# Kernel optimization log

Hardware: AMD Instinct MI355X
Metric: run time of the kernel (lower is better)

Reference implementation:

```python
import jax, jax.numpy as jnp
import numpy as np

EPS = 1e-10


def setup_inputs() -> dict:
    key = jax.random.key(0)
    ks = jax.random.split(key, 8)
    N, C, H, W = 32, 512, 14, 14
    D, HID = 2048, 256
    s1 = 1.0 / np.sqrt(C + D)
    s2 = 1.0 / np.sqrt(HID)
    return {
        "local_feature": jax.random.normal(ks[0], (N, C, H, W), jnp.float32),
        "global_feature": jax.random.normal(ks[1], (N, D, 1, 1), jnp.float32),
        "W1": jax.random.normal(ks[2], (C + D, HID), jnp.float32) * s1,
        "b1": jnp.zeros((HID,), jnp.float32),
        "W2": jax.random.normal(ks[3], (HID, HID), jnp.float32) * s2,
        "b2": jnp.zeros((HID,), jnp.float32),
        "W3": jax.random.normal(ks[4], (HID, 1), jnp.float32) * s2,
        "b3": jnp.zeros((1,), jnp.float32),
    }


def reference(local_feature, global_feature, W1, b1, W2, b2, W3, b3):
    # Vectorized form of DMIEstimator.calculate_mi (the per-sample Python loop
    # collapsed into one batched pass with a block-diagonal negative mask).
    N, C, H, W = local_feature.shape
    hw = H * W
    nhw = N * hw
    D = global_feature.shape[1]

    lf = jnp.transpose(local_feature, (0, 2, 3, 1)).reshape(nhw, C)   # [nhw, C]
    gf = global_feature[:, :, 0, 0]                                   # [N, D]

    # combined = cat([global, local], -1); split the first Linear accordingly
    # so the [N*nhw, C+D] concat tensor is never materialized.
    h_loc = lf @ W1[D:]                        # [nhw, HID]
    h_glb = gf @ W1[:D] + b1                   # [N, HID]
    h1 = jax.nn.relu(h_glb[:, None, :] + h_loc[None, :, :])  # [N, nhw, HID]
    h2 = jax.nn.relu(h1 @ W2 + b2)                            # [N, nhw, HID]
    scores = (h2 @ W3)[..., 0] + b3[0]                        # [N, nhw]

    mx = jnp.max(scores, axis=1, keepdims=True)               # [N, 1]
    ex = jnp.exp(scores - mx)

    # negatives for sample i exclude its own hw block [hw*i, hw*(i+1))
    own = (jnp.arange(nhw)[None, :] // hw) == jnp.arange(N)[:, None]  # [N, nhw]
    neg_mean = jnp.where(own, 0.0, ex).sum(axis=1) / (nhw - hw) + EPS  # [N]

    # positive (diagonal) block of scores: scores[i, hw*i : hw*(i+1)]
    pos = scores.reshape(N, N, hw)[jnp.arange(N), jnp.arange(N)]       # [N, hw]

    mi = pos - mx - jnp.log(neg_mean)[:, None]                         # [N, hw]
    return mi.reshape(N, H, W)
```

## Files before the change

### kernel.cpp

```cpp
#include <hip/hip_runtime.h>
#include <math.h>

#define NB   32
#define CC   512
#define DD   2048
#define HWP  196
#define NHW  6272
#define HID  256

typedef _Float16 h8 __attribute__((ext_vector_type(8)));
typedef _Float16 h4 __attribute__((ext_vector_type(4)));
typedef float    f4 __attribute__((ext_vector_type(4)));
union F4H8 { f4 f; h8 h; };

__device__ __forceinline__ int fragIdx(int j, int k) {
    return ((j >> 6) << 14) + (((k >> 5) * 4 + ((j & 63) >> 4)) << 9)
         + (((((k >> 3) & 3) << 4) + (j & 15)) << 3) + (k & 7);
}

__global__ __launch_bounds__(1024) void prep_kernel(const float* __restrict__ lf,
                                                    const float* __restrict__ gf,
                                                    const float* __restrict__ W1,
                                                    const float* __restrict__ b1,
                                                    const float* __restrict__ W2,
                                                    _Float16* __restrict__ g16,
                                                    _Float16* __restrict__ W2F,
                                                    _Float16* __restrict__ W1F,
                                                    _Float16* __restrict__ lf16T) {
    int bid = blockIdx.x, tid = threadIdx.x;
    if (bid < 32) {
        __shared__ float sP[4][HID];
        int i = bid, k = tid & 255, rc = tid >> 8;
        const float* g = gf + (size_t)i * DD;
        int r0 = rc * 512;
        float acc = 0.f;
        #pragma unroll 8
        for (int r = 0; r < 512; r++)
            acc = fmaf(g[r0 + r], W1[(size_t)(r0 + r) * HID + k], acc);
        sP[rc][k] = acc;
        __syncthreads();
        if (tid < HID)
            g16[(size_t)i * HID + tid] =
                (_Float16)(b1[tid] + sP[0][tid] + sP[1][tid] + sP[2][tid] + sP[3][tid]);
    } else if (bid < 56) {
        int tg = (bid - 32) * 1024 + tid;
        if (tg < 8192) {
            int t = tg, F = t >> 6, l = t & 63;
            int k2t = F >> 3, ks = F & 7;
            int kb = ks * 32 + (l >> 4) * 8;
            int n  = k2t * 16 + (l & 15);
            _Float16* o = W2F + (size_t)t * 8;
            #pragma unroll
            for (int j = 0; j < 8; j++) o[j] = (_Float16)W2[(size_t)(kb + j) * HID + n];
        } else {
            int t = tg - 8192, F = t >> 6, l = t & 63;
            int k2t = F >> 4, ks = F & 15;
            int kb = ks * 32 + (l >> 4) * 8;
            int n  = k2t * 16 + (l & 15);
            const float* W1c = W1 + (size_t)DD * HID;
            _Float16* o = W1F + (size_t)t * 8;
            #pragma unroll
            for (int j = 0; j < 8; j++) o[j] = (_Float16)W1c[(size_t)(kb + j) * HID + n];
        }
    } else {
        __shared__ _Float16 sT[64][HWP + 4];
        int b = bid - 56;
        int n = b >> 1, half = b & 1;
        for (int cb = 0; cb < 4; cb++) {
            int c0 = half * 256 + cb * 64;
            for (int task = tid; task < 64 * 49; task += 1024) {
                int c = task / 49, f = task - c * 49;
                f4 v = *(const f4*)&lf[((size_t)n * CC + c0 + c) * HWP + f * 4];
                h4 o = { (_Float16)v.x, (_Float16)v.y, (_Float16)v.z, (_Float16)v.w };
                *(h4*)&sT[c][f * 4] = o;
            }
            __syncthreads();
            for (int task = tid; task < HWP * 8; task += 1024) {
                int p = task >> 3, ch = task & 7;
                h8 o;
                #pragma unroll
                for (int cc = 0; cc < 8; cc++) o[cc] = sT[ch * 8 + cc][p];
                *(h8*)&lf16T[((size_t)(n * HWP + p)) * CC + c0 + ch * 8] = o;
            }
            __syncthreads();
        }
    }
}

__global__ __launch_bounds__(256, 2) void hlocF_kernel(const _Float16* __restrict__ lf16T,
                                                       const _Float16* __restrict__ W1F,
                                                       _Float16* __restrict__ hF) {
    __shared__ _Float16 sLf[32][CC + 16];
    int tid = threadIdx.x;
    int w = tid >> 6, l = tid & 63, quad = l >> 4, ln = l & 15;
    int j0 = blockIdx.x * 32;
    int khalf = blockIdx.y;

    #pragma unroll
    for (int s = 0; s < 8; s++) {
        int y = s * 256 + tid;
        int row = y >> 6, col = (y & 63) * 8;
        h8 v = *(const h8*)&lf16T[(size_t)(j0 + row) * CC + col];
        *(h8*)&sLf[row][col] = v;
    }

    F4H8 Af[32];
    {
        const f4* src = (const f4*)W1F + l;
        #pragma unroll
        for (int mt = 0; mt < 2; mt++)
            #pragma unroll
            for (int ks = 0; ks < 16; ks++)
                Af[mt * 16 + ks].f = src[(size_t)((khalf * 8 + w * 2 + mt) * 16 + ks) * 64];
    }
    __syncthreads();

    f4 acc[4] = {};
    #pragma unroll
    for (int ks = 0; ks < 16; ks++) {
        h8 bF[2];
        #pragma unroll
        for (int nt = 0; nt < 2; nt++)
            bF[nt] = *(const h8*)&sLf[nt * 16 + ln][ks * 32 + quad * 8];
        #pragma unroll
        for (int mt = 0; mt < 2; mt++)
            #pragma unroll
            for (int nt = 0; nt < 2; nt++)
                acc[mt * 2 + nt] = __builtin_amdgcn_mfma_f32_16x16x32_f16(Af[mt * 16 + ks].h, bF[nt], acc[mt * 2 + nt], 0, 0, 0);
    }

    #pragma unroll
    for (int mt = 0; mt < 2; mt++)
        #pragma unroll
        for (int nt = 0; nt < 2; nt++)
            #pragma unroll
            for (int r = 0; r < 4; r++) {
                int j  = j0 + nt * 16 + ln;
                int k2 = khalf * 128 + w * 32 + mt * 16 + quad * 4 + r;
                hF[fragIdx(j, k2)] = (_Float16)acc[mt * 2 + nt][r];
            }
}

__global__ __launch_bounds__(256, 2) void score_kernel(const _Float16* __restrict__ hF,
                                                       const _Float16* __restrict__ g16,
                                                       const _Float16* __restrict__ W2F,
                                                       const float* __restrict__ b2,
                                                       const float* __restrict__ W3,
                                                       const float* __restrict__ b3,
                                                       float* __restrict__ scores) {
    __shared__ _Float16 sA[64 * HID];
    __shared__ float sRed[64][4];
    int tid = threadIdx.x, w = tid >> 6, l = tid & 63, quad = l >> 4, ln = l & 15;
    int bid = blockIdx.x;
    int i = bid & 31, jt = bid >> 5;

    F4H8 Af[32];
    {
        const f4* src = (const f4*)W2F + l;
        #pragma unroll
        for (int mt = 0; mt < 4; mt++)
            #pragma unroll
            for (int ks = 0; ks < 8; ks++)
                Af[mt * 8 + ks].f = src[(size_t)((w * 4 + mt) * 8 + ks) * 64];
    }

    {
        const _Float16* hbase = hF + (size_t)jt * 16384;
        const _Float16* gbase = g16 + (size_t)i * HID;
        h8 z = {};
        #pragma unroll
        for (int s = 0; s < 8; s++) {
            int y = s * 256 + tid;
            h8 hv = *(const h8*)&hbase[y * 8];
            h8 gq = *(const h8*)&gbase[s * 32 + ((tid >> 4) & 3) * 8];
            h8 hz = __builtin_elementwise_max(hv + gq, z);
            *(h8*)&sA[y * 8] = hz;
        }
    }
    __syncthreads();

    f4 acc[16];
    #pragma unroll
    for (int mt = 0; mt < 4; mt++) {
        f4 bv = *(const f4*)&b2[w * 64 + mt * 16 + quad * 4];
        #pragma unroll
        for (int nt = 0; nt < 4; nt++) acc[mt * 4 + nt] = bv;
    }

    #pragma unroll
    for (int ks = 0; ks < 8; ks++) {
        #pragma unroll
        for (int nt = 0; nt < 4; nt++) {
            h8 hz = *(const h8*)&sA[(ks * 4 + nt) * 512 + l * 8];
            #pragma unroll
            for (int mt = 0; mt < 4; mt++)
                acc[mt * 4 + nt] = __builtin_amdgcn_mfma_f32_16x16x32_f16(Af[mt * 8 + ks].h, hz, acc[mt * 4 + nt], 0, 0, 0);
        }
    }

    #pragma unroll
    for (int nt = 0; nt < 4; nt++) {
        float s = 0.f;
        #pragma unroll
        for (int mt = 0; mt < 4; mt++) {
            f4 w3v = *(const f4*)&W3[w * 64 + mt * 16 + quad * 4];
            s += fmaxf(acc[mt * 4 + nt][0], 0.f) * w3v.x
               + fmaxf(acc[mt * 4 + nt][1], 0.f) * w3v.y
               + fmaxf(acc[mt * 4 + nt][2], 0.f) * w3v.z
               + fmaxf(acc[mt * 4 + nt][3], 0.f) * w3v.w;
        }
        s += __shfl_xor(s, 16, 64);
        s += __shfl_xor(s, 32, 64);
        if (quad == 0) sRed[nt * 16 + ln][w] = s;
    }
    __syncthreads();
    if (tid < 64) {
        f4 v = *(const f4*)&sRed[tid][0];
        scores[(size_t)i * NHW + jt * 64 + tid] = v.x + v.y + v.z + v.w + b3[0];
    }
}

__global__ __launch_bounds__(1024) void reduce_kernel(const float* __restrict__ scores,
                                                      float* __restrict__ out) {
    int i = blockIdx.x, tid = threadIdx.x;
    const float* row = scores + (size_t)i * NHW;
    const f4* row4 = (const f4*)row;
    __shared__ float sW[16], sW2[16], sval[2];
    float mx = -1e30f;
    for (int q = tid; q < 1568; q += 1024) {
        f4 v = row4[q];
        mx = fmaxf(mx, fmaxf(fmaxf(v.x, v.y), fmaxf(v.z, v.w)));
    }
    #pragma unroll
    for (int off = 32; off > 0; off >>= 1) mx = fmaxf(mx, __shfl_down(mx, off, 64));
    if ((tid & 63) == 0) sW[tid >> 6] = mx;
    __syncthreads();
    if (tid == 0) {
        float m = sW[0];
        for (int c = 1; c < 16; c++) m = fmaxf(m, sW[c]);
        sval[0] = m;
    }
    __syncthreads();
    mx = sval[0];
    int q0 = i * 49, q1 = q0 + 49;
    float tot = 0.f, ownv = 0.f;
    for (int q = tid; q < 1568; q += 1024) {
        f4 v = row4[q];
        float e = expf(v.x - mx) + expf(v.y - mx) + expf(v.z - mx) + expf(v.w - mx);
        tot += e;
        if (q >= q0 && q < q1) ownv += e;
    }
    #pragma unroll
    for (int off = 32; off > 0; off >>= 1) {
        tot  += __shfl_down(tot, off, 64);
        ownv += __shfl_down(ownv, off, 64);
    }
    if ((tid & 63) == 0) { sW[tid >> 6] = tot; sW2[tid >> 6] = ownv; }
    __syncthreads();
    if (tid == 0) {
        float t = 0.f, o = 0.f;
        for (int c = 0; c < 16; c++) { t += sW[c]; o += sW2[c]; }
        float neg_mean = (t - o) / (float)(NHW - HWP) + 1e-10f;
        sval[1] = mx + logf(neg_mean);
    }
    __syncthreads();
    float sub = sval[1];
    if (tid < HWP) out[(size_t)i * HWP + tid] = row[i * HWP + tid] - sub;
}

extern "C" void kernel_launch(void* const* d_in, const int* in_sizes, int n_in,
                              void* d_out, int out_size, void* d_ws, size_t ws_size,
                              hipStream_t stream) {
    const float* lf = (const float*)d_in[0];
    const float* gf = (const float*)d_in[1];
    const float* W1 = (const float*)d_in[2];
    const float* b1 = (const float*)d_in[3];
    const float* W2 = (const float*)d_in[4];
    const float* b2 = (const float*)d_in[5];
    const float* W3 = (const float*)d_in[6];
    const float* b3 = (const float*)d_in[7];
    float* out = (float*)d_out;

    char* ws = (char*)d_ws;
    _Float16* hF     = (_Float16*)ws;
    _Float16* g16    = (_Float16*)(ws + 3211264);
    _Float16* W2F    = (_Float16*)(ws + 3227648);
    _Float16* W1F    = (_Float16*)(ws + 3358720);
    _Float16* lf16T  = (_Float16*)(ws + 3620864);
    float*    scores = (float*)   (ws + 10043392);

    hipLaunchKernelGGL(prep_kernel, dim3(120), dim3(1024), 0, stream,
                       lf, gf, W1, b1, W2, g16, W2F, W1F, lf16T);
    hipLaunchKernelGGL(hlocF_kernel, dim3(196, 2), dim3(256), 0, stream, lf16T, W1F, hF);
    hipLaunchKernelGGL(score_kernel, dim3(3136), dim3(256), 0, stream,
                       hF, g16, W2F, b2, W3, b3, scores);
    hipLaunchKernelGGL(reduce_kernel, dim3(NB), dim3(1024), 0, stream, scores, out);
}
```

Before: 145.2 us.

## Split prep work into many small blocks and defer global GEMV reduction

The prep kernel goes from 120 blocks of 1024 threads to 864 blocks of 256 threads. The global-feature GEMV is split into 16 K-chunks per sample that write partial sums to a workspace buffer. An extra block column in the hlocF kernel then sums those partials with b1 into g16. The transpose work is also split per 64-channel slice, and score_kernel's launch bounds are raised to ask for 4 blocks per SM. The aim is to spread the serial prep phase across more CUs; the cost is an extra partial-sum buffer and possible register pressure in score_kernel.

```diff
diff --git a/kernel.cpp b/kernel.cpp
--- a/kernel.cpp
+++ b/kernel.cpp
@@ -18,32 +18,25 @@
          + (((((k >> 3) & 3) << 4) + (j & 15)) << 3) + (k & 7);
 }
 
-__global__ __launch_bounds__(1024) void prep_kernel(const float* __restrict__ lf,
-                                                    const float* __restrict__ gf,
-                                                    const float* __restrict__ W1,
-                                                    const float* __restrict__ b1,
-                                                    const float* __restrict__ W2,
-                                                    _Float16* __restrict__ g16,
-                                                    _Float16* __restrict__ W2F,
-                                                    _Float16* __restrict__ W1F,
-                                                    _Float16* __restrict__ lf16T) {
+__global__ __launch_bounds__(256) void prep_kernel(const float* __restrict__ lf,
+                                                   const float* __restrict__ gf,
+                                                   const float* __restrict__ W1,
+                                                   const float* __restrict__ W2,
+                                                   float* __restrict__ hpart,
+                                                   _Float16* __restrict__ W2F,
+                                                   _Float16* __restrict__ W1F,
+                                                   _Float16* __restrict__ lf16T) {
     int bid = blockIdx.x, tid = threadIdx.x;
-    if (bid < 32) {
-        __shared__ float sP[4][HID];
-        int i = bid, k = tid & 255, rc = tid >> 8;
-        const float* g = gf + (size_t)i * DD;
-        int r0 = rc * 512;
+    if (bid < 512) {
+        int i = bid >> 4, ky = bid & 15, k = tid;
+        const float* g = gf + (size_t)i * DD + ky * 128;
+        const float* w = W1 + (size_t)(ky * 128) * HID + k;
         float acc = 0.f;
         #pragma unroll 8
-        for (int r = 0; r < 512; r++)
-            acc = fmaf(g[r0 + r], W1[(size_t)(r0 + r) * HID + k], acc);
-        sP[rc][k] = acc;
-        __syncthreads();
-        if (tid < HID)
-            g16[(size_t)i * HID + tid] =
-                (_Float16)(b1[tid] + sP[0][tid] + sP[1][tid] + sP[2][tid] + sP[3][tid]);
-    } else if (bid < 56) {
-        int tg = (bid - 32) * 1024 + tid;
+        for (int r = 0; r < 128; r++) acc = fmaf(g[r], w[(size_t)r * HID], acc);
+        hpart[((size_t)i * 16 + ky) * HID + k] = acc;
+    } else if (bid < 608) {
+        int tg = (bid - 512) * 256 + tid;
         if (tg < 8192) {
             int t = tg, F = t >> 6, l = t & 63;
             int k2t = F >> 3, ks = F & 7;
@@ -64,32 +57,42 @@
         }
     } else {
         __shared__ _Float16 sT[64][HWP + 4];
-        int b = bid - 56;
-        int n = b >> 1, half = b & 1;
-        for (int cb = 0; cb < 4; cb++) {
-            int c0 = half * 256 + cb * 64;
-            for (int task = tid; task < 64 * 49; task += 1024) {
-                int c = task / 49, f = task - c * 49;
-                f4 v = *(const f4*)&lf[((size_t)n * CC + c0 + c) * HWP + f * 4];
-                h4 o = { (_Float16)v.x, (_Float16)v.y, (_Float16)v.z, (_Float16)v.w };
-                *(h4*)&sT[c][f * 4] = o;
-            }
-            __syncthreads();
-            for (int task = tid; task < HWP * 8; task += 1024) {
-                int p = task >> 3, ch = task & 7;
-                h8 o;
-                #pragma unroll
-                for (int cc = 0; cc < 8; cc++) o[cc] = sT[ch * 8 + cc][p];
-                *(h8*)&lf16T[((size_t)(n * HWP + p)) * CC + c0 + ch * 8] = o;
-            }
-            __syncthreads();
+        int b = bid - 608;
+        int n = b >> 3, c0 = (b & 7) * 64;
+        for (int task = tid; task < 64 * 49; task += 256) {
+            int c = task / 49, f = task - c * 49;
+            f4 v = *(const f4*)&lf[((size_t)n * CC + c0 + c) * HWP + f * 4];
+            h4 o = { (_Float16)v.x, (_Float16)v.y, (_Float16)v.z, (_Float16)v.w };
+            *(h4*)&sT[c][f * 4] = o;
+        }
+        __syncthreads();
+        for (int task = tid; task < 8 * HWP; task += 256) {
+            int ch = task / HWP, p = task - ch * HWP;
+            h8 o;
+            #pragma unroll
+            for (int cc = 0; cc < 8; cc++) o[cc] = sT[ch * 8 + cc][p];
+            *(h8*)&lf16T[((size_t)(n * HWP + p)) * CC + c0 + ch * 8] = o;
         }
     }
 }
 
 __global__ __launch_bounds__(256, 2) void hlocF_kernel(const _Float16* __restrict__ lf16T,
                                                        const _Float16* __restrict__ W1F,
+                                                       const float* __restrict__ hpart,
+                                                       const float* __restrict__ b1,
+                                                       _Float16* __restrict__ g16,
                                                        _Float16* __restrict__ hF) {
+    if (blockIdx.x == 196) {
+        int kh = blockIdx.y;
+        for (int x = threadIdx.x; x < 16 * HID; x += 256) {
+            int i = kh * 16 + (x >> 8), k = x & 255;
+            float s = b1[k];
+            #pragma unroll
+            for (int ky = 0; ky < 16; ky++) s += hpart[((size_t)i * 16 + ky) * HID + k];
+            g16[(size_t)i * HID + k] = (_Float16)s;
+        }
+        return;
+    }
     __shared__ _Float16 sLf[32][CC + 16];
     int tid = threadIdx.x;
     int w = tid >> 6, l = tid & 63, quad = l >> 4, ln = l & 15;
@@ -141,7 +144,7 @@
             }
 }
 
-__global__ __launch_bounds__(256, 2) void score_kernel(const _Float16* __restrict__ hF,
+__global__ __launch_bounds__(256, 4) void score_kernel(const _Float16* __restrict__ hF,
                                                        const _Float16* __restrict__ g16,
                                                        const _Float16* __restrict__ W2F,
                                                        const float* __restrict__ b2,
@@ -288,10 +291,12 @@
     _Float16* W1F    = (_Float16*)(ws + 3358720);
     _Float16* lf16T  = (_Float16*)(ws + 3620864);
     float*    scores = (float*)   (ws + 10043392);
-
-    hipLaunchKernelGGL(prep_kernel, dim3(120), dim3(1024), 0, stream,
-                       lf, gf, W1, b1, W2, g16, W2F, W1F, lf16T);
-    hipLaunchKernelGGL(hlocF_kernel, dim3(196, 2), dim3(256), 0, stream, lf16T, W1F, hF);
+    float*    hpart  = (float*)   (ws + 10846208);
+
+    hipLaunchKernelGGL(prep_kernel, dim3(864), dim3(256), 0, stream,
+                       lf, gf, W1, W2, hpart, W2F, W1F, lf16T);
+    hipLaunchKernelGGL(hlocF_kernel, dim3(197, 2), dim3(256), 0, stream,
+                       lf16T, W1F, hpart, b1, g16, hF);
     hipLaunchKernelGGL(score_kernel, dim3(3136), dim3(256), 0, stream,
                        hF, g16, W2F, b2, W3, b3, scores);
     hipLaunchKernelGGL(reduce_kernel, dim3(NB), dim3(1024), 0, stream, scores, out);
```

After: 170.3 us. +17.2%, slower.
